# Performance work log

Measured on AMD Instinct MI355X. Metric: run time of the kernel, lower is better.

## Reference

```python
import jax, jax.numpy as jnp
import numpy as np

EPS = 1e-7  # keras.backend.epsilon()


def setup_inputs() -> dict:
    key = jax.random.key(0)
    k1, k2, k3 = jax.random.split(key, 3)
    B, N, D_in, C, D_out = 32, 2048, 8, 32, 16
    x = jax.random.normal(k1, (B, N, D_in), dtype=jnp.float32)
    W = jax.random.normal(k2, (1, N, C, D_out, D_in), dtype=jnp.float32) * 0.05
    R = jax.random.normal(k3, (1, N, C), dtype=jnp.float32)
    return {"x": x, "W": W, "R": R}


def reference(x, W, R):
    # x: [B, N, D_in]; W: [1, N, C, D_out, D_in]; R: [1, N, C]
    R_nor = jax.nn.softmax(R[0], axis=0)          # softmax over N (axis=1 of [1,N,C])
    # per-capsule transform: u[b,n,c,j] = sum_k W[n,c,j,k] * x[b,n,k]
    u = jnp.einsum('ncjk,bnk->bncj', W[0], x)
    # routing-weighted aggregation over input capsules n
    s = jnp.einsum('bncj,nc->bcj', u, R_nor)      # [B, C, D_out]
    # squash along capsule dim (original axis=-2 before squeeze == D_out)
    ss = jnp.sum(jnp.square(s), axis=-1, keepdims=True) + EPS
    scale = jnp.sqrt(ss) / (1.0 + ss)
    return scale * s                               # [B, C, D_out]
```

## Files before the change

kernel.cpp:

```cpp
#include <hip/hip_runtime.h>
#include <math.h>


#define NN 2048
#define CC 32

__device__ __forceinline__ void g2l16(const float* g, float* l) {
  __builtin_amdgcn_global_load_lds((const __attribute__((address_space(1))) void*)g,
                                   (__attribute__((address_space(3))) void*)l, 16, 0, 0);
}

__global__ void __launch_bounds__(512) caps_main(const float* __restrict__ x,
                                                 const float* __restrict__ W,
                                                 const float* __restrict__ R,
                                                 float* __restrict__ P) {
  const int bid = blockIdx.x;
  const int cq = bid >> 6;
  const int chunk = bid & 63;
  const int n0 = chunk * 32;
  const int tid = threadIdx.x;
  const int ws = tid >> 6;
  const int lane = tid & 63;
  const int j = lane & 15;
  const int bo = lane >> 4;

  extern __shared__ float smem[];
  float* ldsW = smem;
  float* ldsX = smem + 8192;
  float* wW = ldsW + ws * 1024;
  float* wX = ldsX + ws * 1024;
  const int nw = n0 + ws * 4;

  float4 rq[4];
#pragma unroll
  for (int nl = 0; nl < 4; ++nl)
    rq[nl] = *(const float4*)(R + (size_t)(nw + nl) * CC + cq * 4);

  auto stageW = [&](int nl, int buf) {
#pragma unroll
    for (int i = 0; i < 2; ++i) {
      int S = i * 64 + lane;
      int g = S ^ (((S >> 2) ^ (S >> 4)) & 1) ^ (((S >> 3) & 1) << 1) ^ (((S >> 4) & 1) << 2);
      g2l16(W + (size_t)(nw + nl) * 4096 + cq * 512 + g * 4, wW + buf * 512 + i * 256);
    }
  };

  stageW(0, 0);
  {
    int g2 = lane ^ ((lane >> 4) << 1);
    int b = g2 >> 1, kq = g2 & 1;
    const float* xs = x + (size_t)b * (NN * 8) + kq * 4;
#pragma unroll
    for (int nl = 0; nl < 4; ++nl)
      g2l16(xs + (size_t)(nw + nl) * 8, wX + nl * 256);
  }
  stageW(1, 1);

  float rv[4][4];
#pragma unroll
  for (int nl = 0; nl < 4; ++nl) {
    rv[nl][0] = expf(rq[nl].x);
    rv[nl][1] = expf(rq[nl].y);
    rv[nl][2] = expf(rq[nl].z);
    rv[nl][3] = expf(rq[nl].w);
  }

  float acc[4][8];
#pragma unroll
  for (int a = 0; a < 4; ++a)
#pragma unroll
    for (int b = 0; b < 8; ++b) acc[a][b] = 0.f;

  const int jsw = j >> 1;

  auto compute = [&](int nl, int buf) {
    const float* Wn = wW + buf * 512;
    const float* Xn = wX + nl * 256;
#pragma unroll
    for (int kh = 0; kh < 2; ++kh) {
      float4 xv[8];
#pragma unroll
      for (int bi = 0; bi < 8; ++bi) {
        int G = (bo * 8 + bi) * 2 + kh;
        int S = G ^ ((G >> 4) << 1);
        xv[bi] = *(const float4*)(Xn + S * 4);
      }
#pragma unroll
      for (int ci = 0; ci < 4; ++ci) {
        int slot = (ci * 32 + j * 2 + kh) ^ jsw;
        float4 wf = *(const float4*)(Wn + slot * 4);
        float rvv = rv[nl][ci];
        float w0 = wf.x * rvv, w1 = wf.y * rvv, w2 = wf.z * rvv, w3 = wf.w * rvv;
#pragma unroll
        for (int bi = 0; bi < 8; ++bi) {
          float a = acc[ci][bi];
          a = fmaf(w0, xv[bi].x, a);
          a = fmaf(w1, xv[bi].y, a);
          a = fmaf(w2, xv[bi].z, a);
          a = fmaf(w3, xv[bi].w, a);
          acc[ci][bi] = a;
        }
      }
    }
  };

  asm volatile("s_waitcnt vmcnt(2)" ::: "memory");
  __builtin_amdgcn_sched_barrier(0);
  compute(0, 0);
  __builtin_amdgcn_sched_barrier(0);
  stageW(2, 0);
  asm volatile("s_waitcnt vmcnt(2)" ::: "memory");
  __builtin_amdgcn_sched_barrier(0);
  compute(1, 1);
  __builtin_amdgcn_sched_barrier(0);
  stageW(3, 1);
  asm volatile("s_waitcnt vmcnt(2)" ::: "memory");
  __builtin_amdgcn_sched_barrier(0);
  compute(2, 0);
  asm volatile("s_waitcnt vmcnt(0)" ::: "memory");
  __builtin_amdgcn_sched_barrier(0);
  compute(3, 1);

#pragma unroll
  for (int ci = 0; ci < 4; ++ci)
#pragma unroll
    for (int bi = 0; bi < 8; ++bi) {
      int cell = (ci * 8 + bi) * 64 + lane;
      float* dst = (ci < 2) ? (ldsW + ws * 1024 + cell)
                            : (ldsX + ws * 1024 + (cell - 1024));
      *dst = acc[ci][bi];
    }
  __syncthreads();
  {
    const int t4 = tid * 4;
    const bool lo = (t4 < 1024);
    float4 ssum = make_float4(0.f, 0.f, 0.f, 0.f);
#pragma unroll
    for (int w = 0; w < 8; ++w) {
      const float* src = lo ? (ldsW + w * 1024 + t4) : (ldsX + w * 1024 + (t4 - 1024));
      float4 v = *(const float4*)src;
      ssum.x += v.x; ssum.y += v.y; ssum.z += v.z; ssum.w += v.w;
    }
    *(float4*)(P + (size_t)bid * 2048 + t4) = ssum;
  }
}

__global__ void caps_reduce(const float* __restrict__ P, const float* __restrict__ R,
                            float* __restrict__ out) {
  const int t = threadIdx.x;
  const int bid = blockIdx.x;

  __shared__ float red[256];
  __shared__ float invd[16];
  {
    const int cl = t & 15, nf = t >> 4;
    const int c0 = (bid * 16) & 31;
    float s = 0.f;
#pragma unroll 16
    for (int i = 0; i < 128; ++i)
      s += expf(R[(size_t)(nf + i * 16) * CC + c0 + cl]);
    red[t] = s;
  }
  __syncthreads();
#pragma unroll
  for (int h = 8; h >= 1; h >>= 1) {
    if ((t >> 4) < h) red[t] += red[t + h * 16];
    __syncthreads();
  }
  if (t < 16) invd[t] = 1.0f / red[t];
  __syncthreads();

  const int g = bid * 256 + t;
  const int j = g & 15;
  const int c = (g >> 4) & 31;
  const int b = g >> 9;
  const int bo = b >> 3, bi = b & 7;
  const int cq = c >> 2, ci = c & 3;
  const int idx = (ci * 8 + bi) * 64 + (bo * 16 + j);
  const float* Pq = P + (size_t)cq * 64 * 2048 + idx;

  float s = 0.f;
#pragma unroll 16
  for (int ch = 0; ch < 64; ++ch)
    s += Pq[(size_t)ch * 2048];
  s *= invd[t >> 4];

  float sq = s * s;
  sq += __shfl_xor(sq, 8, 16);
  sq += __shfl_xor(sq, 4, 16);
  sq += __shfl_xor(sq, 2, 16);
  sq += __shfl_xor(sq, 1, 16);
  float ss = sq + 1e-7f;
  float scale = sqrtf(ss) / (1.0f + ss);
  out[g] = scale * s;
}

extern "C" void kernel_launch(void* const* d_in, const int* in_sizes, int n_in,
                              void* d_out, int out_size, void* d_ws, size_t ws_size,
                              hipStream_t stream) {
  const float* x = (const float*)d_in[0];
  const float* W = (const float*)d_in[1];
  const float* R = (const float*)d_in[2];
  float* out = (float*)d_out;
  float* P = (float*)d_ws;

  hipFuncSetAttribute((const void*)caps_main,
                      hipFuncAttributeMaxDynamicSharedMemorySize, 65536);

  caps_main<<<512, 512, 65536, stream>>>(x, W, R, P);
  caps_reduce<<<64, 256, 0, stream>>>(P, R, out);
}
```

Before: 28.39 us.

## Triple-buffer W staging per wave and vectorize final reduce kernel

The main kernel now keeps three W buffers per wave instead of two, issuing three W prefetches up front so more global-to-LDS loads are in flight while computing. The per-wave LDS region is reorganized into a single contiguous block reused for the cross-wave partial-sum reduction, which raises dynamic LDS to 80KB. The reduce kernel is restructured to one block per capsule with float4 loads of partials, a wave-shuffle softmax denominator, and float4 output stores. The larger LDS footprint may reduce how many blocks fit per CU.

```diff
diff --git a/kernel.cpp b/kernel.cpp
--- a/kernel.cpp
+++ b/kernel.cpp
@@ -25,16 +25,16 @@
   const int bo = lane >> 4;
 
   extern __shared__ float smem[];
-  float* ldsW = smem;
-  float* ldsX = smem + 8192;
-  float* wW = ldsW + ws * 1024;
-  float* wX = ldsX + ws * 1024;
+  float* wREG = smem + ws * 2560;
+  float* wW = wREG;
+  float* wX = wREG + 1536;
   const int nw = n0 + ws * 4;
 
   float4 rq[4];
 #pragma unroll
   for (int nl = 0; nl < 4; ++nl)
     rq[nl] = *(const float4*)(R + (size_t)(nw + nl) * CC + cq * 4);
+  __builtin_amdgcn_sched_barrier(0);
 
   auto stageW = [&](int nl, int buf) {
 #pragma unroll
@@ -46,6 +46,7 @@
   };
 
   stageW(0, 0);
+  __builtin_amdgcn_sched_barrier(0);
   {
     int g2 = lane ^ ((lane >> 4) << 1);
     int b = g2 >> 1, kq = g2 & 1;
@@ -54,7 +55,11 @@
     for (int nl = 0; nl < 4; ++nl)
       g2l16(xs + (size_t)(nw + nl) * 8, wX + nl * 256);
   }
+  __builtin_amdgcn_sched_barrier(0);
   stageW(1, 1);
+  __builtin_amdgcn_sched_barrier(0);
+  stageW(2, 2);
+  __builtin_amdgcn_sched_barrier(0);
 
   float rv[4][4];
 #pragma unroll
@@ -104,41 +109,35 @@
     }
   };
 
+  asm volatile("s_waitcnt vmcnt(4)" ::: "memory");
+  __builtin_amdgcn_sched_barrier(0);
+  compute(0, 0);
+  asm volatile("s_waitcnt lgkmcnt(0)" ::: "memory");
+  __builtin_amdgcn_sched_barrier(0);
+  stageW(3, 0);
+  __builtin_amdgcn_sched_barrier(0);
+  asm volatile("s_waitcnt vmcnt(4)" ::: "memory");
+  __builtin_amdgcn_sched_barrier(0);
+  compute(1, 1);
   asm volatile("s_waitcnt vmcnt(2)" ::: "memory");
   __builtin_amdgcn_sched_barrier(0);
-  compute(0, 0);
-  __builtin_amdgcn_sched_barrier(0);
-  stageW(2, 0);
-  asm volatile("s_waitcnt vmcnt(2)" ::: "memory");
-  __builtin_amdgcn_sched_barrier(0);
-  compute(1, 1);
-  __builtin_amdgcn_sched_barrier(0);
-  stageW(3, 1);
-  asm volatile("s_waitcnt vmcnt(2)" ::: "memory");
-  __builtin_amdgcn_sched_barrier(0);
-  compute(2, 0);
+  compute(2, 2);
   asm volatile("s_waitcnt vmcnt(0)" ::: "memory");
   __builtin_amdgcn_sched_barrier(0);
-  compute(3, 1);
+  compute(3, 0);
 
 #pragma unroll
   for (int ci = 0; ci < 4; ++ci)
 #pragma unroll
-    for (int bi = 0; bi < 8; ++bi) {
-      int cell = (ci * 8 + bi) * 64 + lane;
-      float* dst = (ci < 2) ? (ldsW + ws * 1024 + cell)
-                            : (ldsX + ws * 1024 + (cell - 1024));
-      *dst = acc[ci][bi];
-    }
+    for (int bi = 0; bi < 8; ++bi)
+      wREG[(ci * 8 + bi) * 64 + lane] = acc[ci][bi];
   __syncthreads();
   {
     const int t4 = tid * 4;
-    const bool lo = (t4 < 1024);
     float4 ssum = make_float4(0.f, 0.f, 0.f, 0.f);
 #pragma unroll
     for (int w = 0; w < 8; ++w) {
-      const float* src = lo ? (ldsW + w * 1024 + t4) : (ldsX + w * 1024 + (t4 - 1024));
-      float4 v = *(const float4*)src;
+      float4 v = *(const float4*)(smem + (size_t)w * 2560 + t4);
       ssum.x += v.x; ssum.y += v.y; ssum.z += v.z; ssum.w += v.w;
     }
     *(float4*)(P + (size_t)bid * 2048 + t4) = ssum;
@@ -147,52 +146,44 @@
 
 __global__ void caps_reduce(const float* __restrict__ P, const float* __restrict__ R,
                             float* __restrict__ out) {
+  const int c = blockIdx.x;
   const int t = threadIdx.x;
-  const int bid = blockIdx.x;
-
-  __shared__ float red[256];
-  __shared__ float invd[16];
+  const int b = t >> 2, jq = t & 3;
+
+  __shared__ float red[2];
   {
-    const int cl = t & 15, nf = t >> 4;
-    const int c0 = (bid * 16) & 31;
     float s = 0.f;
+#pragma unroll
+    for (int i = 0; i < 16; ++i)
+      s += expf(R[(size_t)(t + i * 128) * CC + c]);
+#pragma unroll
+    for (int d = 32; d >= 1; d >>= 1) s += __shfl_xor(s, d, 64);
+    if ((t & 63) == 0) red[t >> 6] = s;
+  }
+  __syncthreads();
+  const float inv = 1.0f / (red[0] + red[1]);
+
+  const int cq = c >> 2, ci = c & 3;
+  const int bo = b >> 3, bi = b & 7;
+  const int cell = (ci * 8 + bi) * 64 + bo * 16 + jq * 4;
+  const float* Pq = P + (size_t)cq * 64 * 2048 + cell;
+
+  float4 s4 = make_float4(0.f, 0.f, 0.f, 0.f);
 #pragma unroll 16
-    for (int i = 0; i < 128; ++i)
-      s += expf(R[(size_t)(nf + i * 16) * CC + c0 + cl]);
-    red[t] = s;
-  }
-  __syncthreads();
-#pragma unroll
-  for (int h = 8; h >= 1; h >>= 1) {
-    if ((t >> 4) < h) red[t] += red[t + h * 16];
-    __syncthreads();
-  }
-  if (t < 16) invd[t] = 1.0f / red[t];
-  __syncthreads();
-
-  const int g = bid * 256 + t;
-  const int j = g & 15;
-  const int c = (g >> 4) & 31;
-  const int b = g >> 9;
-  const int bo = b >> 3, bi = b & 7;
-  const int cq = c >> 2, ci = c & 3;
-  const int idx = (ci * 8 + bi) * 64 + (bo * 16 + j);
-  const float* Pq = P + (size_t)cq * 64 * 2048 + idx;
-
-  float s = 0.f;
-#pragma unroll 16
-  for (int ch = 0; ch < 64; ++ch)
-    s += Pq[(size_t)ch * 2048];
-  s *= invd[t >> 4];
-
-  float sq = s * s;
-  sq += __shfl_xor(sq, 8, 16);
-  sq += __shfl_xor(sq, 4, 16);
-  sq += __shfl_xor(sq, 2, 16);
-  sq += __shfl_xor(sq, 1, 16);
+  for (int ch = 0; ch < 64; ++ch) {
+    float4 v = *(const float4*)(Pq + (size_t)ch * 2048);
+    s4.x += v.x; s4.y += v.y; s4.z += v.z; s4.w += v.w;
+  }
+  s4.x *= inv; s4.y *= inv; s4.z *= inv; s4.w *= inv;
+
+  float sq = s4.x * s4.x + s4.y * s4.y + s4.z * s4.z + s4.w * s4.w;
+  sq += __shfl_xor(sq, 1, 4);
+  sq += __shfl_xor(sq, 2, 4);
   float ss = sq + 1e-7f;
   float scale = sqrtf(ss) / (1.0f + ss);
-  out[g] = scale * s;
+  s4.x *= scale; s4.y *= scale; s4.z *= scale; s4.w *= scale;
+
+  *(float4*)(out + (size_t)b * 512 + c * 16 + jq * 4) = s4;
 }
 
 extern "C" void kernel_launch(void* const* d_in, const int* in_sizes, int n_in,
@@ -205,8 +196,8 @@
   float* P = (float*)d_ws;
 
   hipFuncSetAttribute((const void*)caps_main,
-                      hipFuncAttributeMaxDynamicSharedMemorySize, 65536);
-
-  caps_main<<<512, 512, 65536, stream>>>(x, W, R, P);
-  caps_reduce<<<64, 256, 0, stream>>>(P, R, out);
-}
+                      hipFuncAttributeMaxDynamicSharedMemorySize, 81920);
+
+  caps_main<<<512, 512, 81920, stream>>>(x, W, R, P);
+  caps_reduce<<<32, 128, 0, stream>>>(P, R, out);
+}
```

After: 27.09 us (median of 2 runs). 4.6% less time.
